# Kernel optimization log

Measured on AMD Instinct MI355X. Metric: run time of the kernel, lower is better.

## Reference

```python
import jax, jax.numpy as jnp
import numpy as np

G = 5   # grid intervals
K = 3   # spline order
D_MODEL, D_FF = 512, 2048
B, S = 2, 2048

def make_grid():
    h = 2.0 / G
    # extended knot vector: G + 2K + 1 points spanning [-1 - K*h, 1 + K*h]
    return (jnp.arange(-K, G + K + 1, dtype=jnp.float32) * h - 1.0)

def b_splines(x, grid, k):
    # x: (N, in), grid: (G+2k+1,) -> bases: (N, in, G+k) via Cox-de Boor
    x = x[..., None]  # (N, in, 1)
    bases = ((x >= grid[:-1]) & (x < grid[1:])).astype(x.dtype)  # order-0, (N,in,G+2k)
    for j in range(1, k + 1):
        left = (x - grid[: -(j + 1)]) / (grid[j:-1] - grid[: -(j + 1)])
        right = (grid[j + 1:] - x) / (grid[j + 1:] - grid[1:-j])
        bases = left * bases[..., :-1] + right * bases[..., 1:]
    return bases

def kan_layer(x, grid, w_base, w_spline):
    # x: (N, in); w_base: (out, in); w_spline: (out, in, G+k)
    base = jax.nn.silu(x) @ w_base.T                      # residual base path
    bases = b_splines(x, grid, K)                          # (N, in, G+k)
    spline = jnp.einsum('nig,oig->no', bases, w_spline)    # per-edge spline contraction
    return base + spline

def setup_inputs() -> dict:
    key = jax.random.key(0)
    ks = jax.random.split(key, 5)
    sc1 = 1.0 / np.sqrt(D_MODEL)
    sc2 = 1.0 / np.sqrt(D_FF)
    return {
        'x': jax.random.normal(ks[0], (B, S, D_MODEL), dtype=jnp.float32),
        'grid': make_grid(),
        'w1_base': jax.random.normal(ks[1], (D_FF, D_MODEL), dtype=jnp.float32) * sc1,
        'w1_spline': jax.random.normal(ks[2], (D_FF, D_MODEL, G + K), dtype=jnp.float32) * (0.1 * sc1),
        'w2_base': jax.random.normal(ks[3], (D_MODEL, D_FF), dtype=jnp.float32) * sc2,
        'w2_spline': jax.random.normal(ks[4], (D_MODEL, D_FF, G + K), dtype=jnp.float32) * (0.1 * sc2),
    }

def reference(x, grid, w1_base, w1_spline, w2_base, w2_spline):
    b, s, d = x.shape
    xf = x.reshape(-1, d)                      # (N, d_model)
    h = kan_layer(xf, grid, w1_base, w1_spline)   # (N, d_ff)
    out = kan_layer(h, grid, w2_base, w2_spline)  # (N, d_model)
    return out.reshape(b, s, d)
```

## Files before the change

kernel.cpp:

```cpp
#include <hip/hip_runtime.h>
#include <stdint.h>


typedef __bf16 bf16x8_t __attribute__((ext_vector_type(8)));
typedef float f32x4_t __attribute__((ext_vector_type(4)));

__device__ __forceinline__ float bf2f(unsigned short u) {
    union { float f; uint32_t i; } c; c.i = ((uint32_t)u) << 16; return c.f;
}
__device__ __forceinline__ unsigned short f2bf(float f) {
    union { float f; uint32_t u; } c; c.f = f;
    uint32_t u = c.u;
    u += 0x7FFFu + ((u >> 16) & 1u);
    return (unsigned short)(u >> 16);
}
__device__ __forceinline__ bool f32world(const void* gridp) {
    return ((*(const unsigned int*)gridp) & 0xFFFFu) == 0xCCCDu;
}

__device__ __forceinline__ void load_knots(const void* gridp, float* t, float* rr) {
    if (f32world(gridp)) {
        const float* g = (const float*)gridp;
#pragma unroll
        for (int k = 0; k < 12; ++k) t[k] = g[k];
    } else {
        const unsigned short* g = (const unsigned short*)gridp;
#pragma unroll
        for (int k = 0; k < 12; ++k) t[k] = bf2f(g[k]);
    }
    rr[0] = 1.0f / (t[1] - t[0]);
    rr[1] = 1.0f / (t[2] - t[0]);
    rr[2] = 1.0f / (t[3] - t[0]);
}

__device__ __forceinline__ int4 bases8(float x, const float* t, const float* rr) {
    float b[11];
#pragma unroll
    for (int j = 0; j < 11; ++j)
        b[j] = (x >= t[j] && x < t[j + 1]) ? 1.0f : 0.0f;
#pragma unroll
    for (int j = 1; j <= 3; ++j) {
        float inv = rr[j - 1];
#pragma unroll
        for (int i = 0; i + j < 11; ++i) {
            float left  = (x - t[i]) * inv;
            float right = (t[i + j + 1] - x) * inv;
            b[i] = left * b[i] + right * b[i + 1];
        }
    }
    union { int4 v; unsigned short h[8]; } u;
#pragma unroll
    for (int g = 0; g < 8; ++g) u.h[g] = f2bf(b[g]);
    return u.v;
}

__global__ __launch_bounds__(256)
void cvt4_kernel(const void* __restrict__ s0, const void* __restrict__ s1,
                 const void* __restrict__ s2, const void* __restrict__ s3,
                 unsigned short* __restrict__ dst, const void* __restrict__ gridp)
{
    const int n0 = 262144;
    const int n01 = n0 + 2097152;
    const int n012 = n01 + 262144;
    const int n = n012 + 2097152;
    int i = blockIdx.x * 256 + threadIdx.x;
    if (i >= n) return;
    const void* src; long off;
    if      (i < n0)   { src = s0; off = i; }
    else if (i < n01)  { src = s1; off = i - n0; }
    else if (i < n012) { src = s2; off = i - n01; }
    else               { src = s3; off = i - n012; }
    if (f32world(gridp)) {
        float4 v = ((const float4*)src)[off];
        ushort4 o;
        o.x = f2bf(v.x); o.y = f2bf(v.y); o.z = f2bf(v.z); o.w = f2bf(v.w);
        ((ushort4*)dst)[i] = o;
    } else {
        ((ushort4*)dst)[i] = ((const ushort4*)src)[off];
    }
}

template<int XMODE>
__global__ __launch_bounds__(256)
void act_kernel(const void* __restrict__ Xv, const void* __restrict__ gridp,
                unsigned short* __restrict__ S, unsigned short* __restrict__ BS,
                int total4, float* __restrict__ zbuf, int zn4)
{
    int gi = blockIdx.x * 256 + threadIdx.x;
    if (gi >= total4) return;

    if (zbuf && gi < zn4) ((float4*)zbuf)[gi] = (float4){0.f, 0.f, 0.f, 0.f};

    const bool w32 = f32world(gridp);
    float t[12], rr[3];
    load_knots(gridp, t, rr);

    float xv[4];
    if (XMODE == 0 && w32) {
        float4 v = ((const float4*)Xv)[gi];
        xv[0] = v.x; xv[1] = v.y; xv[2] = v.z; xv[3] = v.w;
    } else {
        ushort4 v = ((const ushort4*)Xv)[gi];
        xv[0] = bf2f(v.x); xv[1] = bf2f(v.y); xv[2] = bf2f(v.z); xv[3] = bf2f(v.w);
    }

    ushort4 sOut;
    unsigned short* sp = (unsigned short*)&sOut;
    int4 bsOut[4];

#pragma unroll
    for (int e = 0; e < 4; ++e) {
        float x = xv[e];
        float sg = 1.0f / (1.0f + __expf(-x));
        sp[e] = f2bf(x * sg);
        bsOut[e] = bases8(x, t, rr);
    }

    ((ushort4*)S)[gi] = sOut;
    int4* bp = (int4*)&BS[(long)gi * 32];
#pragma unroll
    for (int e = 0; e < 4; ++e) bp[e] = bsOut[e];
}

template<int BM, int BN, int OUT_MODE>
__global__ __launch_bounds__(256)
void gemm_seg(const unsigned short* __restrict__ A0, int K0,
              const unsigned short* __restrict__ A1, int K1,
              const unsigned short* __restrict__ B0,
              const unsigned short* __restrict__ B1,
              void* __restrict__ Cv, unsigned short* __restrict__ BSp,
              int N, int crow0, int ktiles,
              const void* __restrict__ gridp)
{
    constexpr int BK = 64;
    constexpr int TM = BM / 32;
    constexpr int TN = BN / 32;

    __shared__ unsigned short As[BM * BK];
    __shared__ unsigned short Bs[BN * BK];

    const int tid  = threadIdx.x;
    const int lane = tid & 63;
    const int w    = tid >> 6;
    const int wm   = w & 1;
    const int wn   = w >> 1;

    const int gx = gridDim.x, gy = gridDim.y, gz = gridDim.z;
    int bx = blockIdx.x, by = blockIdx.y, bz = blockIdx.z;
    {
        int NB = gx * gy * gz;
        if ((NB & 7) == 0) {
            int F = bx + gx * (by + gy * bz);
            int T = (F & 7) * (NB >> 3) + (F >> 3);
            int pl = gx * gy;
            bz = T / pl;
            int r = T - bz * pl;
            by = r / gx;
            bx = r - by * gx;
        }
    }

    const int rowA0 = by * BM;
    const int colC0 = bx * BN;

    const int nkt0 = K0 / BK;
    const int nkt  = nkt0 + K1 / BK;
    const int kt0  = bz * ktiles;
    const int kt1  = (kt0 + ktiles < nkt) ? kt0 + ktiles : nkt;

    const int srow = (w << 3) + (lane >> 3);
    const int scol = (((lane & 7) ^ ((lane >> 3) & 7)) << 3);

    const int q  = lane >> 4;
    const int l7 = lane & 7;
    const int cidx0 = ((q) ^ l7) << 3;
    const int cidx1 = ((4 + q) ^ l7) << 3;

    f32x4_t acc[TM][TN];
#pragma unroll
    for (int i = 0; i < TM; ++i)
#pragma unroll
        for (int j = 0; j < TN; ++j)
            acc[i][j] = (f32x4_t){0.f, 0.f, 0.f, 0.f};

    for (int kt = kt0; kt < kt1; ++kt) {
        const unsigned short* Abase;
        const unsigned short* Bbase;
        long ld; int ko;
        if (kt < nkt0) { Abase = A0; Bbase = B0; ld = K0; ko = kt * BK; }
        else           { Abase = A1; Bbase = B1; ld = K1; ko = (kt - nkt0) * BK; }

#pragma unroll
        for (int i = 0; i < BM / 32; ++i) {
            const unsigned short* g = Abase + (long)(rowA0 + i * 32 + srow) * ld + ko + scol;
            __builtin_amdgcn_global_load_lds(
                (const __attribute__((address_space(1))) void*)g,
                (__attribute__((address_space(3))) void*)&As[(i * 32 + (w << 3)) * BK],
                16, 0, 0);
        }
#pragma unroll
        for (int i = 0; i < BN / 32; ++i) {
            const unsigned short* g = Bbase + (long)(colC0 + i * 32 + srow) * ld + ko + scol;
            __builtin_amdgcn_global_load_lds(
                (const __attribute__((address_space(1))) void*)g,
                (__attribute__((address_space(3))) void*)&Bs[(i * 32 + (w << 3)) * BK],
                16, 0, 0);
        }
        __syncthreads();

#pragma unroll
        for (int ks = 0; ks < 2; ++ks) {
            const int cidx = ks ? cidx1 : cidx0;
            bf16x8_t af[TM], bfr[TN];
#pragma unroll
            for (int tm = 0; tm < TM; ++tm)
                af[tm] = *(const bf16x8_t*)&As[(wm * (BM / 2) + tm * 16 + (lane & 15)) * BK
                                               + cidx];
#pragma unroll
            for (int tn = 0; tn < TN; ++tn)
                bfr[tn] = *(const bf16x8_t*)&Bs[(wn * (BN / 2) + tn * 16 + (lane & 15)) * BK
                                                + cidx];
#pragma unroll
            for (int tm = 0; tm < TM; ++tm)
#pragma unroll
                for (int tn = 0; tn < TN; ++tn)
                    acc[tm][tn] = __builtin_amdgcn_mfma_f32_16x16x32_bf16(
                        af[tm], bfr[tn], acc[tm][tn], 0, 0, 0);
        }
        __syncthreads();
    }

    const bool w32 = (OUT_MODE == 2) ? f32world(gridp) : false;
    float t[12], rr[3];
    if (OUT_MODE == 3) load_knots(gridp, t, rr);

#pragma unroll
    for (int tm = 0; tm < TM; ++tm) {
#pragma unroll
        for (int tn = 0; tn < TN; ++tn) {
            int row0 = crow0 + rowA0 + wm * (BM / 2) + tm * 16 + (lane >> 4) * 4;
            int col  = colC0 + wn * (BN / 2) + tn * 16 + (lane & 15);
#pragma unroll
            for (int r = 0; r < 4; ++r) {
                long off = (long)(row0 + r) * N + col;
                float v = acc[tm][tn][r];
                if (OUT_MODE == 1) {
                    unsafeAtomicAdd(&((float*)Cv)[off], v);
                } else if (OUT_MODE == 3) {
                    float sg = 1.0f / (1.0f + __expf(-v));
                    ((unsigned short*)Cv)[off] = f2bf(v * sg);
                    *(int4*)&BSp[off * 8] = bases8(v, t, rr);
                } else if (w32) {
                    ((float*)Cv)[off] = v;
                } else {
                    ((unsigned short*)Cv)[off] = f2bf(v);
                }
            }
        }
    }
}

__global__ __launch_bounds__(256)
void accum_to_out(const float* __restrict__ acc, void* __restrict__ out,
                  int n4, const void* __restrict__ gridp)
{
    int i = blockIdx.x * 256 + threadIdx.x;
    if (i >= n4) return;
    float4 v = ((const float4*)acc)[i];
    if (f32world(gridp)) {
        ((float4*)out)[i] = v;
    } else {
        ushort4 o;
        o.x = f2bf(v.x); o.y = f2bf(v.y); o.z = f2bf(v.z); o.w = f2bf(v.w);
        ((ushort4*)out)[i] = o;
    }
}

extern "C" void kernel_launch(void* const* d_in, const int* in_sizes, int n_in,
                              void* d_out, int out_size, void* d_ws, size_t ws_size,
                              hipStream_t stream)
{
    const void* x   = d_in[0];
    const void* grd = d_in[1];
    const void* w1b = d_in[2];
    const void* w1s = d_in[3];
    const void* w2b = d_in[4];
    const void* w2s = d_in[5];

    const int NTOK = 4096, D1 = 512, D2 = 2048;
    const size_t MiB = 1024 * 1024;
    char* ws = (char*)d_ws;

    if (ws_size >= 224 * MiB) {
        unsigned short* wcat   = (unsigned short*)ws;
        unsigned short* w1b_bf = (unsigned short*)(ws);
        unsigned short* w1s_bf = (unsigned short*)(ws + 2  * MiB);
        unsigned short* w2b_bf = (unsigned short*)(ws + 18 * MiB);
        unsigned short* w2s_bf = (unsigned short*)(ws + 20 * MiB);
        unsigned short* S1     = (unsigned short*)(ws + 36 * MiB);
        unsigned short* BS1    = (unsigned short*)(ws + 40 * MiB);
        unsigned short* S2     = (unsigned short*)(ws + 72 * MiB);
        unsigned short* BS2    = (unsigned short*)(ws + 88 * MiB);
        float*          C2     = (float*)(ws + 216 * MiB);

        cvt4_kernel<<<(4718592 + 255) / 256, 256, 0, stream>>>(w1b, w1s, w2b, w2s, wcat, grd);

        act_kernel<0><<<(NTOK * D1 / 4 + 255) / 256, 256, 0, stream>>>(
            x, grd, S1, BS1, NTOK * D1 / 4, (float*)C2, NTOK * D1 / 4);

        {
            dim3 g(D2 / 128, NTOK / 64, 1);
            gemm_seg<64, 128, 3><<<g, 256, 0, stream>>>(
                S1, D1, BS1, D1 * 8, w1b_bf, w1s_bf,
                (void*)S2, BS2, D2, 0, 72, grd);
        }

        {
            dim3 g(D1 / 128, NTOK / 128, 8);
            gemm_seg<128, 128, 1><<<g, 256, 0, stream>>>(
                S2, D2, BS2, D2 * 8, w2b_bf, w2s_bf,
                (void*)C2, nullptr, D1, 0, 36, grd);
        }

        accum_to_out<<<(NTOK * D1 / 4 + 255) / 256, 256, 0, stream>>>(
            C2, d_out, NTOK * D1 / 4, grd);
    } else {
        unsigned short* w1b_bf = (unsigned short*)(ws);
        unsigned short* w1s_bf = (unsigned short*)(ws + 2  * MiB);
        unsigned short* w2b_bf = (unsigned short*)(ws + 18 * MiB);
        unsigned short* w2s_bf = (unsigned short*)(ws + 20 * MiB);
        unsigned short* H      = (unsigned short*)(ws + 36 * MiB);
        unsigned short* S1     = (unsigned short*)(ws + 52 * MiB);
        unsigned short* BS1    = (unsigned short*)(ws + 56 * MiB);
        unsigned short* S2     = (unsigned short*)(ws + 52 * MiB);
        unsigned short* BS2    = (unsigned short*)(ws + 68 * MiB);

        int CT;
        if      (ws_size >= 100 * MiB) CT = 1024;
        else                           CT = 256;

        cvt4_kernel<<<(4718592 + 255) / 256, 256, 0, stream>>>(
            w1b, w1s, w2b, w2s, (unsigned short*)ws, grd);

        {
            act_kernel<0><<<(NTOK * D1 / 4 + 255) / 256, 256, 0, stream>>>(
                x, grd, S1, BS1, NTOK * D1 / 4, nullptr, 0);
            dim3 g(D2 / 128, NTOK / 128, 1);
            gemm_seg<128, 128, 2><<<g, 256, 0, stream>>>(
                S1, D1, BS1, D1 * 8, w1b_bf, w1s_bf, (void*)H, nullptr,
                D2, 0, 72, grd);
        }
        int nch = NTOK / CT;
        for (int c = 0; c < nch; ++c) {
            long tokOff = (long)c * CT;
            act_kernel<1><<<(CT * D2 / 4 + 255) / 256, 256, 0, stream>>>(
                (const void*)(H + tokOff * D2), grd, S2 + tokOff * D2, BS2,
                CT * D2 / 4, nullptr, 0);
            dim3 g(D1 / 128, CT / 64, 1);
            gemm_seg<64, 128, 2><<<g, 256, 0, stream>>>(
                S2 + tokOff * D2, D2, BS2, D2 * 8, w2b_bf, w2s_bf,
                d_out, nullptr, D1, (int)tokOff, 288, grd);
        }
    }
}
```

Measured before the change: 402.3 us.

## Compute SiLU and B-spline bases of hidden activations on the fly in second GEMM

The first GEMM now writes only the raw hidden activation H in bf16, instead of also writing the SiLU and 8-wide B-spline basis tensors. The second GEMM reads H directly and computes SiLU or the spline bases while staging A tiles into shared memory, replacing the async global-to-LDS copy. This removes a large write and read of the 8x-expanded basis tensor. In exchange, basis computation is repeated for every N-tile and split-K block, and A loads go through registers instead of direct LDS loads.

```diff
diff --git a/kernel.cpp b/kernel.cpp
--- a/kernel.cpp
+++ b/kernel.cpp
@@ -122,7 +122,7 @@
     for (int e = 0; e < 4; ++e) bp[e] = bsOut[e];
 }
 
-template<int BM, int BN, int OUT_MODE>
+template<int BM, int BN, int OUT_MODE, int AMODE = 0>
 __global__ __launch_bounds__(256)
 void gemm_seg(const unsigned short* __restrict__ A0, int K0,
               const unsigned short* __restrict__ A1, int K1,
@@ -176,6 +176,9 @@
     const int cidx0 = ((q) ^ l7) << 3;
     const int cidx1 = ((4 + q) ^ l7) << 3;
 
+    float t[12], rr[3];
+    if (OUT_MODE == 3 || AMODE == 1) load_knots(gridp, t, rr);
+
     f32x4_t acc[TM][TN];
 #pragma unroll
     for (int i = 0; i < TM; ++i)
@@ -184,19 +187,56 @@
             acc[i][j] = (f32x4_t){0.f, 0.f, 0.f, 0.f};
 
     for (int kt = kt0; kt < kt1; ++kt) {
-        const unsigned short* Abase;
+        const bool seg0 = (kt < nkt0);
         const unsigned short* Bbase;
         long ld; int ko;
-        if (kt < nkt0) { Abase = A0; Bbase = B0; ld = K0; ko = kt * BK; }
-        else           { Abase = A1; Bbase = B1; ld = K1; ko = (kt - nkt0) * BK; }
-
-#pragma unroll
-        for (int i = 0; i < BM / 32; ++i) {
-            const unsigned short* g = Abase + (long)(rowA0 + i * 32 + srow) * ld + ko + scol;
-            __builtin_amdgcn_global_load_lds(
-                (const __attribute__((address_space(1))) void*)g,
-                (__attribute__((address_space(3))) void*)&As[(i * 32 + (w << 3)) * BK],
-                16, 0, 0);
+        if (seg0) { Bbase = B0; ld = K0; ko = kt * BK; }
+        else      { Bbase = B1; ld = K1; ko = (kt - nkt0) * BK; }
+
+        if (AMODE == 0) {
+            const unsigned short* Abase = seg0 ? A0 : A1;
+#pragma unroll
+            for (int i = 0; i < BM / 32; ++i) {
+                const unsigned short* g = Abase + (long)(rowA0 + i * 32 + srow) * ld + ko + scol;
+                __builtin_amdgcn_global_load_lds(
+                    (const __attribute__((address_space(1))) void*)g,
+                    (__attribute__((address_space(3))) void*)&As[(i * 32 + (w << 3)) * BK],
+                    16, 0, 0);
+            }
+        } else {
+            const int s = lane & 7;
+            const int c = s ^ (srow & 7);
+            if (seg0) {
+#pragma unroll
+                for (int i = 0; i < BM / 32; ++i) {
+                    const int row = rowA0 + i * 32 + srow;
+                    ushort4 h0 = *(const ushort4*)(A0 + (long)row * K0 + ko + c * 8);
+                    ushort4 h1 = *(const ushort4*)(A0 + (long)row * K0 + ko + c * 8 + 4);
+                    ushort4 o0, o1;
+                    {
+                        float xx, sg;
+                        xx = bf2f(h0.x); sg = 1.0f / (1.0f + __expf(-xx)); o0.x = f2bf(xx * sg);
+                        xx = bf2f(h0.y); sg = 1.0f / (1.0f + __expf(-xx)); o0.y = f2bf(xx * sg);
+                        xx = bf2f(h0.z); sg = 1.0f / (1.0f + __expf(-xx)); o0.z = f2bf(xx * sg);
+                        xx = bf2f(h0.w); sg = 1.0f / (1.0f + __expf(-xx)); o0.w = f2bf(xx * sg);
+                        xx = bf2f(h1.x); sg = 1.0f / (1.0f + __expf(-xx)); o1.x = f2bf(xx * sg);
+                        xx = bf2f(h1.y); sg = 1.0f / (1.0f + __expf(-xx)); o1.y = f2bf(xx * sg);
+                        xx = bf2f(h1.z); sg = 1.0f / (1.0f + __expf(-xx)); o1.z = f2bf(xx * sg);
+                        xx = bf2f(h1.w); sg = 1.0f / (1.0f + __expf(-xx)); o1.w = f2bf(xx * sg);
+                    }
+                    unsigned short* dst = &As[(i * 32 + srow) * BK + s * 8];
+                    *(ushort4*)dst = o0;
+                    *(ushort4*)(dst + 4) = o1;
+                }
+            } else {
+#pragma unroll
+                for (int i = 0; i < BM / 32; ++i) {
+                    const int row = rowA0 + i * 32 + srow;
+                    float hval = bf2f(A0[(long)row * K0 + (ko >> 3) + c]);
+                    int4 val = bases8(hval, t, rr);
+                    *(int4*)&As[(i * 32 + srow) * BK + s * 8] = val;
+                }
+            }
         }
 #pragma unroll
         for (int i = 0; i < BN / 32; ++i) {
@@ -231,8 +271,6 @@
     }
 
     const bool w32 = (OUT_MODE == 2) ? f32world(gridp) : false;
-    float t[12], rr[3];
-    if (OUT_MODE == 3) load_knots(gridp, t, rr);
 
 #pragma unroll
     for (int tm = 0; tm < TM; ++tm) {
@@ -250,6 +288,8 @@
                     float sg = 1.0f / (1.0f + __expf(-v));
                     ((unsigned short*)Cv)[off] = f2bf(v * sg);
                     *(int4*)&BSp[off * 8] = bases8(v, t, rr);
+                } else if (OUT_MODE == 4) {
+                    ((unsigned short*)Cv)[off] = f2bf(v);
                 } else if (w32) {
                     ((float*)Cv)[off] = v;
                 } else {
@@ -299,8 +339,7 @@
         unsigned short* w2s_bf = (unsigned short*)(ws + 20 * MiB);
         unsigned short* S1     = (unsigned short*)(ws + 36 * MiB);
         unsigned short* BS1    = (unsigned short*)(ws + 40 * MiB);
-        unsigned short* S2     = (unsigned short*)(ws + 72 * MiB);
-        unsigned short* BS2    = (unsigned short*)(ws + 88 * MiB);
+        unsigned short* H      = (unsigned short*)(ws + 72 * MiB);
         float*          C2     = (float*)(ws + 216 * MiB);
 
         cvt4_kernel<<<(4718592 + 255) / 256, 256, 0, stream>>>(w1b, w1s, w2b, w2s, wcat, grd);
@@ -310,15 +349,15 @@
 
         {
             dim3 g(D2 / 128, NTOK / 64, 1);
-            gemm_seg<64, 128, 3><<<g, 256, 0, stream>>>(
+            gemm_seg<64, 128, 4><<<g, 256, 0, stream>>>(
                 S1, D1, BS1, D1 * 8, w1b_bf, w1s_bf,
-                (void*)S2, BS2, D2, 0, 72, grd);
+                (void*)H, nullptr, D2, 0, 72, grd);
         }
 
         {
             dim3 g(D1 / 128, NTOK / 128, 8);
-            gemm_seg<128, 128, 1><<<g, 256, 0, stream>>>(
-                S2, D2, BS2, D2 * 8, w2b_bf, w2s_bf,
+            gemm_seg<128, 128, 1, 1><<<g, 256, 0, stream>>>(
+                H, D2, H, D2 * 8, w2b_bf, w2s_bf,
                 (void*)C2, nullptr, D1, 0, 36, grd);
         }
 
```

Result: slower. 488.5 us (+21.4%).
